# Performance work log

Hardware: AMD Instinct MI355X
Metric: run time of the kernel (lower is better)

## Reference

```python
import jax, jax.numpy as jnp
import numpy as np

B, N, NDIM = 256, 127, 3          # batch, particles, input features
D, H, L, HID = 256, 8, 4, 256     # d_model, heads, layers, dim_feedforward(=nb_features=head hidden)
M = HID                           # Performer nb_features
DH = D // H                       # head dim
LN_EPS = 1e-5
KERN_EPS = 1e-4


def leaky(x):
    return jnp.where(x >= 0, x, 0.2 * x)


def layer_norm(x, g, b):
    mu = jnp.mean(x, axis=-1, keepdims=True)
    var = jnp.mean((x - mu) ** 2, axis=-1, keepdims=True)
    return (x - mu) * jax.lax.rsqrt(var + LN_EPS) * g + b


def softmax_kernel(data, proj, is_query):
    # FAVOR+ positive softmax random features (performer_pytorch.softmax_kernel)
    # data [B,H,S,DH], proj [M,DH]
    normalizer = DH ** -0.25
    ratio = proj.shape[0] ** -0.5
    dd = jnp.einsum('bhnd,md->bhnm', data * normalizer, proj)
    diag = jnp.sum(data ** 2, axis=-1, keepdims=True) * 0.5 * (normalizer ** 2)
    if is_query:
        mx = jax.lax.stop_gradient(jnp.max(dd, axis=-1, keepdims=True))
    else:
        mx = jax.lax.stop_gradient(jnp.max(dd))
    return ratio * (jnp.exp(dd - diag - mx) + KERN_EPS)


def performer_attn(h, keep, Wq, bq, Wk, bk, Wv, bv, Wo, bo, proj):
    Bc, S, _ = h.shape
    def split(y):
        return y.reshape(Bc, S, H, DH).transpose(0, 2, 1, 3)  # [B,H,S,DH]
    q = split(jnp.einsum('bnd,ed->bne', h, Wq) + bq)
    k = split(jnp.einsum('bnd,ed->bne', h, Wk) + bk)
    v = split(jnp.einsum('bnd,ed->bne', h, Wv) + bv) * keep   # zero padded values
    qp = softmax_kernel(q, proj, True)    # [B,H,S,M]
    kp = softmax_kernel(k, proj, False)   # [B,H,S,M]
    ksum = jnp.sum(kp, axis=2)                                   # [B,H,M]
    d_inv = 1.0 / jnp.einsum('bhnm,bhm->bhn', qp, ksum)          # [B,H,S]
    ctx = jnp.einsum('bhnm,bhnd->bhmd', kp, v)                   # [B,H,M,DH]
    o = jnp.einsum('bhmd,bhnm,bhn->bhnd', ctx, qp, d_inv)
    o = o.transpose(0, 2, 1, 3).reshape(Bc, S, D)
    return jnp.einsum('bnd,ed->bne', o, Wo) + bo


def encoder_layer(h, keep, Wq, bq, Wk, bk, Wv, bv, Wo, bo, proj,
                  n1w, n1b, n2w, n2b, f1w, f1b, f2w, f2b):
    # NOTE: the repo's override drops the residual connections (post-norm, no skip)
    a = performer_attn(h, keep, Wq, bq, Wk, bk, Wv, bv, Wo, bo, proj)
    h = layer_norm(a, n1w, n1b)
    f = jnp.einsum('bnh,dh->bnd', leaky(jnp.einsum('bnd,hd->bnh', h, f1w) + f1b), f2w) + f2b
    return layer_norm(f, n2w, n2b)


def setup_inputs():
    key = jax.random.key(0)
    ks = jax.random.split(key, 32)
    s = 0.02
    def w(k, shape):
        return jax.random.normal(k, shape, jnp.float32) * s
    return {
        'x': jax.random.normal(ks[0], (B, N, NDIM), jnp.float32),
        'mask': jax.random.randint(ks[1], (B, N), 0, 2) == 1,
        'emb_w': w(ks[2], (D, NDIM)), 'emb_b': w(ks[3], (D,)),
        'Wq': w(ks[4], (L, D, D)), 'bq': w(ks[5], (L, D)),
        'Wk': w(ks[6], (L, D, D)), 'bk': w(ks[7], (L, D)),
        'Wv': w(ks[8], (L, D, D)), 'bv': w(ks[9], (L, D)),
        'Wo': w(ks[10], (L, D, D)), 'bo': w(ks[11], (L, D)),
        'proj': jax.random.normal(ks[12], (L, M, DH), jnp.float32),
        'n1w': jnp.ones((L, D)), 'n1b': jnp.zeros((L, D)),
        'n2w': jnp.ones((L, D)), 'n2b': jnp.zeros((L, D)),
        'f1w': w(ks[13], (L, HID, D)), 'f1b': w(ks[14], (L, HID)),
        'f2w': w(ks[15], (L, D, HID)), 'f2b': w(ks[16], (L, D)),
        'h1w': w(ks[17], (2 * HID, D)), 'h1b': w(ks[18], (2 * HID,)),
        'h2w': w(ks[19], (HID, 2 * HID)), 'h2b': w(ks[20], (HID,)),
        'ow': w(ks[21], (1, HID)), 'ob': w(ks[22], (1,)),
    }


def reference(x, mask, emb_w, emb_b, Wq, bq, Wk, bk, Wv, bv, Wo, bo, proj,
              n1w, n1b, n2w, n2b, f1w, f1b, f2w, f2b,
              h1w, h1b, h2w, h2b, ow, ob):
    h = jnp.einsum('bnf,df->bnd', x, emb_w) + emb_b               # embed [B,N,D]
    h = jnp.concatenate([jnp.zeros_like(h[:, :1]), h], axis=1)    # prepend zero CLS token
    pad = jnp.concatenate([jnp.zeros_like(mask[:, :1]), mask], axis=1)  # [B,N+1], True=pad
    keep = (~pad).astype(h.dtype)[:, None, :, None]               # [B,1,S,1]
    for l in range(L):
        h = encoder_layer(h, keep, Wq[l], bq[l], Wk[l], bk[l], Wv[l], bv[l],
                          Wo[l], bo[l], proj[l], n1w[l], n1b[l], n2w[l], n2b[l],
                          f1w[l], f1b[l], f2w[l], f2b[l])
    c = h[:, 0]                                                   # CLS token [B,D]
    c = leaky(jnp.einsum('bd,hd->bh', c, h1w) + h1b)
    c = leaky(jnp.einsum('bh,gh->bg', c, h2w) + h2b)
    return jnp.einsum('bg,og->bo', c, ow) + ob                    # [B,1]
```

## Files before the change

### kernel.cpp

```cpp
#include <hip/hip_runtime.h>
#include <math.h>

#define B_ 256
#define N_ 127
#define S_ 128
#define NDIM_ 3
#define D_ 256
#define H_ 8
#define DH_ 32
#define M_ 256
#define HID_ 256
#define L_ 4
#define LOG2E 1.44269504088896340736f

typedef __attribute__((ext_vector_type(8))) short short8;
typedef __attribute__((ext_vector_type(4))) short bfx4;
typedef __attribute__((ext_vector_type(4))) float floatx4;

__device__ __forceinline__ ushort bf16_rn(float x) {
    unsigned u = __float_as_uint(x);
    u = (u + 0x7fffu + ((u >> 16) & 1u)) >> 16;
    return (ushort)u;
}
__device__ __forceinline__ unsigned split_pack(float x) {
    const ushort h = bf16_rn(x);
    const float r = x - __uint_as_float(((unsigned)h) << 16);
    const ushort l = bf16_rn(r);
    return (unsigned)h | ((unsigned)l << 16);
}
__device__ __forceinline__ float rec(unsigned u) {
    return __uint_as_float(u << 16) + __uint_as_float(u & 0xffff0000u);
}
__device__ __forceinline__ unsigned hpair(unsigned u0, unsigned u1) {
    return (u0 & 0xffffu) | (u1 << 16);
}
__device__ __forceinline__ unsigned lpair(unsigned u0, unsigned u1) {
    return (u0 >> 16) | (u1 & 0xffff0000u);
}

__device__ __forceinline__ float blk_sum(float v, float* sred) {
#pragma unroll
    for (int o = 32; o > 0; o >>= 1) v += __shfl_xor(v, o, 64);
    if ((threadIdx.x & 63) == 0) sred[threadIdx.x >> 6] = v;
    __syncthreads();
    v = sred[0] + sred[1] + sred[2] + sred[3];
    __syncthreads();
    return v;
}

__global__ void __launch_bounds__(256) k_prep(
    const float* __restrict__ Wq, const float* __restrict__ Wk, const float* __restrict__ Wv,
    const float* __restrict__ Wo, const float* __restrict__ f1w, const float* __restrict__ f2w,
    const float* __restrict__ proj, ushort* __restrict__ WH, ushort* __restrict__ WL,
    unsigned* __restrict__ P2, int* __restrict__ slots,
    const float* __restrict__ x, const float* __restrict__ ew, const float* __restrict__ eb,
    unsigned* __restrict__ Aout)
{
    const int bid = blockIdx.x;
    if (bid < 768) {
        const int tensor = bid / 128;
        const int tid = (bid & 127) * 256 + threadIdx.x;
        const float* src = tensor == 0 ? Wq : tensor == 1 ? Wk : tensor == 2 ? Wv
                         : tensor == 3 ? Wo : tensor == 4 ? f1w : f2w;
        ushort* dh = WH + (size_t)tensor * L_ * 65536;
        ushort* dl = WL + (size_t)tensor * L_ * 65536;
        const int l = tid >> 13;
        const int col = (tid >> 5) & 255, kc = tid & 31;
        const float* sp = src + ((size_t)l << 16) + col * 256 + kc * 8;
        float v[8];
        *(float4*)&v[0] = *(const float4*)sp;
        *(float4*)&v[4] = *(const float4*)(sp + 4);
        unsigned hu[4], lu[4];
#pragma unroll
        for (int i = 0; i < 4; i++) {
            const unsigned u0 = split_pack(v[2 * i]);
            const unsigned u1 = split_pack(v[2 * i + 1]);
            hu[i] = hpair(u0, u1);
            lu[i] = lpair(u0, u1);
        }
        const size_t off = ((size_t)l << 16) + ((size_t)(kc * 256 + col)) * 8;
        *(uint4*)&dh[off] = make_uint4(hu[0], hu[1], hu[2], hu[3]);
        *(uint4*)&dl[off] = make_uint4(lu[0], lu[1], lu[2], lu[3]);
    } else if (bid < 800) {
        const int idx = ((bid - 768) * 256 + threadIdx.x) * 4;
        const float4 w4 = *(const float4*)&proj[idx];
        const float v[4] = {w4.x, w4.y, w4.z, w4.w};
        unsigned u[4];
#pragma unroll
        for (int i = 0; i < 4; i++) u[i] = split_pack(v[i]);
        *(uint4*)&P2[idx] = make_uint4(u[0], u[1], u[2], u[3]);
    } else if (bid == 800) {
        if (threadIdx.x < 4) {
            const int i = __float_as_int(-INFINITY);
            slots[threadIdx.x] = (i >= 0) ? i : (i ^ 0x7fffffff);
        }
    } else {
        const int idx4 = (bid - 801) * 256 + threadIdx.x;
        const int d0 = (idx4 & 63) * 4;
        const int n = (idx4 >> 6) & (S_ - 1);
        const int b = idx4 >> 13;
        unsigned r[4] = {0u, 0u, 0u, 0u};
        if (n > 0) {
            const float* xr = x + ((size_t)b * N_ + (n - 1)) * NDIM_;
            const float x0 = xr[0], x1 = xr[1], x2 = xr[2];
#pragma unroll
            for (int j = 0; j < 4; j++) {
                const int d = d0 + j;
                const float val = eb[d] + x0 * ew[d * 3 + 0] + x1 * ew[d * 3 + 1] + x2 * ew[d * 3 + 2];
                r[j] = split_pack(val);
            }
        }
        *(uint4*)&Aout[(size_t)idx4 * 4] = make_uint4(r[0], r[1], r[2], r[3]);
    }
}

template<int EPI>
__global__ void __launch_bounds__(512, 2) k_gemm(
    const unsigned* __restrict__ Ap, const ushort* __restrict__ WH,
    const ushort* __restrict__ WL,
    const float* __restrict__ bias, const float* __restrict__ g1,
    const float* __restrict__ g2, const int* __restrict__ mask,
    unsigned* __restrict__ out)
{
    __shared__ ushort sAh[2][4160];
    __shared__ ushort sAl[2][4160];
    __shared__ float sredA[128][4], sredB[128][4];
    const int t = threadIdx.x;
    const int w = t >> 6, lane = t & 63;
    const int quad = lane >> 4, l16 = lane & 15;
    const int rowbase = 64 * (w >> 2), colbase = 64 * (w & 3);
    const int colg = w & 3;
    const int row0 = blockIdx.x * 128;

    floatx4 acc[4][4];
#pragma unroll
    for (int rt = 0; rt < 4; rt++)
#pragma unroll
        for (int ct = 0; ct < 4; ct++) acc[rt][ct] = (floatx4){0.f, 0.f, 0.f, 0.f};

    const int arow = t >> 2, achunk = t & 3;
    const unsigned* AG = Ap + (size_t)(row0 + arow) * D_ + achunk * 8;
    const int aidx = achunk * 1040 + arow * 8;

    {
        const uint4 a0 = *(const uint4*)AG;
        const uint4 a1 = *(const uint4*)(AG + 4);
        *(uint4*)&sAh[0][aidx] = make_uint4(hpair(a0.x, a0.y), hpair(a0.z, a0.w),
                                            hpair(a1.x, a1.y), hpair(a1.z, a1.w));
        *(uint4*)&sAl[0][aidx] = make_uint4(lpair(a0.x, a0.y), lpair(a0.z, a0.w),
                                            lpair(a1.x, a1.y), lpair(a1.z, a1.w));
    }
    __syncthreads();

    for (int s = 0; s < 8; s++) {
        const int p = s & 1;
        uint4 a0n, a1n;
        if (s + 1 < 8) {
            a0n = *(const uint4*)(AG + (s + 1) * 32);
            a1n = *(const uint4*)(AG + (s + 1) * 32 + 4);
        }
        const size_t wbase = ((size_t)((s * 4 + quad) * 256 + colbase + l16)) * 8;
        const ushort* WHf = WH + wbase;
        const ushort* WLf = WL + wbase;
        short8 ah[4], al[4], wh[4], wl[4];
#pragma unroll
        for (int ct = 0; ct < 4; ct++) {
            wh[ct] = *(const short8*)&WHf[ct * 128];
            wl[ct] = *(const short8*)&WLf[ct * 128];
        }
#pragma unroll
        for (int rt = 0; rt < 4; rt++) {
            const int ai = quad * 1040 + (rowbase + 16 * rt + l16) * 8;
            ah[rt] = *(const short8*)&sAh[p][ai];
            al[rt] = *(const short8*)&sAl[p][ai];
        }
#pragma unroll
        for (int rt = 0; rt < 4; rt++)
#pragma unroll
            for (int ct = 0; ct < 4; ct++) {
                acc[rt][ct] = __builtin_amdgcn_mfma_f32_16x16x32_bf16(ah[rt], wh[ct], acc[rt][ct], 0, 0, 0);
                acc[rt][ct] = __builtin_amdgcn_mfma_f32_16x16x32_bf16(ah[rt], wl[ct], acc[rt][ct], 0, 0, 0);
                acc[rt][ct] = __builtin_amdgcn_mfma_f32_16x16x32_bf16(al[rt], wh[ct], acc[rt][ct], 0, 0, 0);
            }
        if (s + 1 < 8) {
            *(uint4*)&sAh[p ^ 1][aidx] = make_uint4(hpair(a0n.x, a0n.y), hpair(a0n.z, a0n.w),
                                                    hpair(a1n.x, a1n.y), hpair(a1n.z, a1n.w));
            *(uint4*)&sAl[p ^ 1][aidx] = make_uint4(lpair(a0n.x, a0n.y), lpair(a0n.z, a0n.w),
                                                    lpair(a1n.x, a1n.y), lpair(a1n.z, a1n.w));
        }
        __syncthreads();
    }

    int colv[4]; float bv[4];
#pragma unroll
    for (int ct = 0; ct < 4; ct++) { colv[ct] = colbase + 16 * ct + l16; bv[ct] = bias[colv[ct]]; }

    if (EPI <= 1) {
        const int b = row0 >> 7;
#pragma unroll
        for (int rt = 0; rt < 4; rt++)
#pragma unroll
        for (int i = 0; i < 4; i++) {
            const int rl = rowbase + 16 * rt + quad * 4 + i;
            const int n = (row0 + rl) & (S_ - 1);
            float keep = 1.f;
            if (EPI == 1) keep = (n == 0) ? 1.f : (mask[b * N_ + n - 1] ? 0.f : 1.f);
#pragma unroll
            for (int ct = 0; ct < 4; ct++) {
                float c = acc[rt][ct][i] + bv[ct];
                if (EPI == 1) c *= keep;
                const int col = colv[ct];
                out[(((size_t)b * H_ + (col >> 5)) * S_ + n) * DH_ + (col & 31)] = split_pack(c);
            }
        }
    } else if (EPI == 2) {
        float gv[4], bbv[4];
#pragma unroll
        for (int ct = 0; ct < 4; ct++) { gv[ct] = g1[colv[ct]]; bbv[ct] = g2[colv[ct]]; }
#pragma unroll
        for (int rt = 0; rt < 4; rt++)
#pragma unroll
        for (int i = 0; i < 4; i++) {
            const int rl = rowbase + 16 * rt + quad * 4 + i;
            float s = 0.f, s2 = 0.f;
#pragma unroll
            for (int ct = 0; ct < 4; ct++) {
                const float c = acc[rt][ct][i] + bv[ct];
                s += c; s2 += c * c;
            }
#pragma unroll
            for (int o = 8; o > 0; o >>= 1) { s += __shfl_xor(s, o, 64); s2 += __shfl_xor(s2, o, 64); }
            if (l16 == 0) { sredA[rl][colg] = s; sredB[rl][colg] = s2; }
        }
        __syncthreads();
#pragma unroll
        for (int rt = 0; rt < 4; rt++)
#pragma unroll
        for (int i = 0; i < 4; i++) {
            const int rl = rowbase + 16 * rt + quad * 4 + i;
            const float s = sredA[rl][0] + sredA[rl][1] + sredA[rl][2] + sredA[rl][3];
            const float s2 = sredB[rl][0] + sredB[rl][1] + sredB[rl][2] + sredB[rl][3];
            const float mu = s * (1.f / D_);
            const float rs = rsqrtf(s2 * (1.f / D_) - mu * mu + 1e-5f);
#pragma unroll
            for (int ct = 0; ct < 4; ct++) {
                const float c = acc[rt][ct][i] + bv[ct];
                out[(size_t)(row0 + rl) * D_ + colv[ct]] = split_pack((c - mu) * rs * gv[ct] + bbv[ct]);
            }
        }
    } else {
#pragma unroll
        for (int rt = 0; rt < 4; rt++)
#pragma unroll
        for (int i = 0; i < 4; i++) {
            const int rl = rowbase + 16 * rt + quad * 4 + i;
#pragma unroll
            for (int ct = 0; ct < 4; ct++) {
                const float c = acc[rt][ct][i] + bv[ct];
                out[(size_t)(row0 + rl) * D_ + colv[ct]] = split_pack((c >= 0.f) ? c : 0.2f * c);
            }
        }
    }
}

__global__ void __launch_bounds__(512, 2) k_gemm_qkv(
    const unsigned* __restrict__ Ap, const ushort* __restrict__ WHb,
    const ushort* __restrict__ WLb, const int l,
    const float* __restrict__ bq, const float* __restrict__ bk, const float* __restrict__ bv_,
    const int* __restrict__ mask,
    unsigned* __restrict__ Qo, unsigned* __restrict__ Ko, unsigned* __restrict__ Vo)
{
    __shared__ ushort sAh[2][4160];
    __shared__ ushort sAl[2][4160];
    const int t = threadIdx.x;
    const int w = t >> 6, lane = t & 63;
    const int quad = lane >> 4, l16 = lane & 15;
    const int rowbase = 64 * (w >> 2), colbase = 64 * (w & 3);
    const int which = blockIdx.x >> 8;
    const int row0 = (blockIdx.x & 255) * 128;
    const ushort* WH = WHb + ((size_t)(which * L_ + l)) * 65536;
    const ushort* WL = WLb + ((size_t)(which * L_ + l)) * 65536;
    const float* bias = which == 0 ? bq : which == 1 ? bk : bv_;
    unsigned* out = which == 0 ? Qo : which == 1 ? Ko : Vo;

    floatx4 acc[4][4];
#pragma unroll
    for (int rt = 0; rt < 4; rt++)
#pragma unroll
        for (int ct = 0; ct < 4; ct++) acc[rt][ct] = (floatx4){0.f, 0.f, 0.f, 0.f};

    const int arow = t >> 2, achunk = t & 3;
    const unsigned* AG = Ap + (size_t)(row0 + arow) * D_ + achunk * 8;
    const int aidx = achunk * 1040 + arow * 8;

    {
        const uint4 a0 = *(const uint4*)AG;
        const uint4 a1 = *(const uint4*)(AG + 4);
        *(uint4*)&sAh[0][aidx] = make_uint4(hpair(a0.x, a0.y), hpair(a0.z, a0.w),
                                            hpair(a1.x, a1.y), hpair(a1.z, a1.w));
        *(uint4*)&sAl[0][aidx] = make_uint4(lpair(a0.x, a0.y), lpair(a0.z, a0.w),
                                            lpair(a1.x, a1.y), lpair(a1.z, a1.w));
    }
    __syncthreads();

    for (int s = 0; s < 8; s++) {
        const int p = s & 1;
        uint4 a0n, a1n;
        if (s + 1 < 8) {
            a0n = *(const uint4*)(AG + (s + 1) * 32);
            a1n = *(const uint4*)(AG + (s + 1) * 32 + 4);
        }
        const size_t wbase = ((size_t)((s * 4 + quad) * 256 + colbase + l16)) * 8;
        const ushort* WHf = WH + wbase;
        const ushort* WLf = WL + wbase;
        short8 ah[4], al[4], wh[4], wl[4];
#pragma unroll
        for (int ct = 0; ct < 4; ct++) {
            wh[ct] = *(const short8*)&WHf[ct * 128];
            wl[ct] = *(const short8*)&WLf[ct * 128];
        }
#pragma unroll
        for (int rt = 0; rt < 4; rt++) {
            const int ai = quad * 1040 + (rowbase + 16 * rt + l16) * 8;
            ah[rt] = *(const short8*)&sAh[p][ai];
            al[rt] = *(const short8*)&sAl[p][ai];
        }
#pragma unroll
        for (int rt = 0; rt < 4; rt++)
#pragma unroll
            for (int ct = 0; ct < 4; ct++) {
                acc[rt][ct] = __builtin_amdgcn_mfma_f32_16x16x32_bf16(ah[rt], wh[ct], acc[rt][ct], 0, 0, 0);
                acc[rt][ct] = __builtin_amdgcn_mfma_f32_16x16x32_bf16(ah[rt], wl[ct], acc[rt][ct], 0, 0, 0);
                acc[rt][ct] = __builtin_amdgcn_mfma_f32_16x16x32_bf16(al[rt], wh[ct], acc[rt][ct], 0, 0, 0);
            }
        if (s + 1 < 8) {
            *(uint4*)&sAh[p ^ 1][aidx] = make_uint4(hpair(a0n.x, a0n.y), hpair(a0n.z, a0n.w),
                                                    hpair(a1n.x, a1n.y), hpair(a1n.z, a1n.w));
            *(uint4*)&sAl[p ^ 1][aidx] = make_uint4(lpair(a0n.x, a0n.y), lpair(a0n.z, a0n.w),
                                                    lpair(a1n.x, a1n.y), lpair(a1n.z, a1n.w));
        }
        __syncthreads();
    }

    int colv[4]; float bv[4];
#pragma unroll
    for (int ct = 0; ct < 4; ct++) { colv[ct] = colbase + 16 * ct + l16; bv[ct] = bias[colv[ct]]; }

    const int b = row0 >> 7;
#pragma unroll
    for (int rt = 0; rt < 4; rt++)
#pragma unroll
    for (int i = 0; i < 4; i++) {
        const int rl = rowbase + 16 * rt + quad * 4 + i;
        const int n = (row0 + rl) & (S_ - 1);
        float keep = 1.f;
        if (which == 2) keep = (n == 0) ? 1.f : (mask[b * N_ + n - 1] ? 0.f : 1.f);
#pragma unroll
        for (int ct = 0; ct < 4; ct++) {
            float c = acc[rt][ct][i] + bv[ct];
            c *= keep;
            const int col = colv[ct];
            out[(((size_t)b * H_ + (col >> 5)) * S_ + n) * DH_ + (col & 31)] = split_pack(c);
        }
    }
}

__global__ void __launch_bounds__(512, 4) k_ffn(
    const unsigned* __restrict__ Ap,
    const ushort* __restrict__ W1H, const ushort* __restrict__ W1L,
    const ushort* __restrict__ W2H, const ushort* __restrict__ W2L,
    const float* __restrict__ b1, const float* __restrict__ b2,
    const float* __restrict__ g1, const float* __restrict__ g2,
    unsigned* __restrict__ out)
{
    __shared__ char smemc[67584];
    ushort* h1h = (ushort*)smemc;
    ushort* h1l = (ushort*)(smemc + 33792);
    ushort* sTh = (ushort*)smemc;
    ushort* sTl = (ushort*)(smemc + 8320);
    __shared__ float sredA[64][4], sredB[64][4];
    const int t = threadIdx.x;
    const int w = t >> 6, lane = t & 63;
    const int quad = lane >> 4, l16 = lane & 15;
    const int row0 = blockIdx.x * 64;

    floatx4 acc[2][4];
#pragma unroll
    for (int rt = 0; rt < 2; rt++)
#pragma unroll
        for (int ct = 0; ct < 4; ct++) acc[rt][ct] = (floatx4){0.f, 0.f, 0.f, 0.f};

    const int arow = t >> 3, akq = t & 7;
    const unsigned* AG = Ap + (size_t)(row0 + arow) * D_ + akq * 4;
    const int aidx = (akq >> 1) * 520 + arow * 8 + (akq & 1) * 4;

    {
        const uint4 a4 = *(const uint4*)AG;
        *(uint2*)&sTh[aidx] = make_uint2(hpair(a4.x, a4.y), hpair(a4.z, a4.w));
        *(uint2*)&sTl[aidx] = make_uint2(lpair(a4.x, a4.y), lpair(a4.z, a4.w));
    }
    __syncthreads();

    for (int s = 0; s < 8; s++) {
        const int p = s & 1;
        uint4 a_n;
        if (s + 1 < 8) a_n = *(const uint4*)(AG + (s + 1) * 32);
        const size_t wbase = ((size_t)((s * 4 + quad) * 256 + 32 * w + l16)) * 8;
        short8 fh[2], fl[2], th[4], tl[4];
#pragma unroll
        for (int rt = 0; rt < 2; rt++) {
            fh[rt] = *(const short8*)&W1H[wbase + rt * 128];
            fl[rt] = *(const short8*)&W1L[wbase + rt * 128];
        }
#pragma unroll
        for (int ct = 0; ct < 4; ct++) {
            const int ti = p * 2080 + quad * 520 + (16 * ct + l16) * 8;
            th[ct] = *(const short8*)&sTh[ti];
            tl[ct] = *(const short8*)&sTl[ti];
        }
#pragma unroll
        for (int rt = 0; rt < 2; rt++)
#pragma unroll
            for (int ct = 0; ct < 4; ct++) {
                acc[rt][ct] = __builtin_amdgcn_mfma_f32_16x16x32_bf16(fh[rt], th[ct], acc[rt][ct], 0, 0, 0);
                acc[rt][ct] = __builtin_amdgcn_mfma_f32_16x16x32_bf16(fl[rt], th[ct], acc[rt][ct], 0, 0, 0);
                acc[rt][ct] = __builtin_amdgcn_mfma_f32_16x16x32_bf16(fh[rt], tl[ct], acc[rt][ct], 0, 0, 0);
            }
        if (s + 1 < 8) {
            *(uint2*)&sTh[(p ^ 1) * 2080 + aidx] = make_uint2(hpair(a_n.x, a_n.y), hpair(a_n.z, a_n.w));
            *(uint2*)&sTl[(p ^ 1) * 2080 + aidx] = make_uint2(lpair(a_n.x, a_n.y), lpair(a_n.z, a_n.w));
        }
        __syncthreads();
    }
#pragma unroll
    for (int rt = 0; rt < 2; rt++)
#pragma unroll
    for (int ct = 0; ct < 4; ct++) {
        unsigned u[4];
#pragma unroll
        for (int i = 0; i < 4; i++) {
            const int col2 = 32 * w + 16 * rt + quad * 4 + i;
            float c = acc[rt][ct][i] + b1[col2];
            c = (c >= 0.f) ? c : 0.2f * c;
            u[i] = split_pack(c);
        }
        const int base = (16 * ct + l16) * 264 + 32 * w + 16 * rt + quad * 4;
        *(uint2*)&h1h[base] = make_uint2(hpair(u[0], u[1]), hpair(u[2], u[3]));
        *(uint2*)&h1l[base] = make_uint2(lpair(u[0], u[1]), lpair(u[2], u[3]));
    }
    __syncthreads();

    const int rowbase = 32 * (w >> 2), colbase = 64 * (w & 3);
    const int colg = w & 3;
    floatx4 acc2[2][4];
#pragma unroll
    for (int rt = 0; rt < 2; rt++)
#pragma unroll
        for (int ct = 0; ct < 4; ct++) acc2[rt][ct] = (floatx4){0.f, 0.f, 0.f, 0.f};

    for (int ks = 0; ks < 8; ks++) {
        const size_t w2base = ((size_t)((ks * 4 + quad) * 256 + colbase + l16)) * 8;
        short8 ah[2], al[2], wh[4], wl[4];
#pragma unroll
        for (int ct = 0; ct < 4; ct++) {
            wh[ct] = *(const short8*)&W2H[w2base + ct * 128];
            wl[ct] = *(const short8*)&W2L[w2base + ct * 128];
        }
#pragma unroll
        for (int rt = 0; rt < 2; rt++) {
            const int gi = (rowbase + 16 * rt + l16) * 264 + ks * 32 + quad * 8;
            ah[rt] = *(const short8*)&h1h[gi];
            al[rt] = *(const short8*)&h1l[gi];
        }
#pragma unroll
        for (int rt = 0; rt < 2; rt++)
#pragma unroll
            for (int ct = 0; ct < 4; ct++) {
                acc2[rt][ct] = __builtin_amdgcn_mfma_f32_16x16x32_bf16(ah[rt], wh[ct], acc2[rt][ct], 0, 0, 0);
                acc2[rt][ct] = __builtin_amdgcn_mfma_f32_16x16x32_bf16(ah[rt], wl[ct], acc2[rt][ct], 0, 0, 0);
                acc2[rt][ct] = __builtin_amdgcn_mfma_f32_16x16x32_bf16(al[rt], wh[ct], acc2[rt][ct], 0, 0, 0);
            }
    }
    __syncthreads();

    int colv[4]; float bv[4], gv[4], bbv[4];
#pragma unroll
    for (int ct = 0; ct < 4; ct++) {
        colv[ct] = colbase + 16 * ct + l16;
        bv[ct] = b2[colv[ct]];
        gv[ct] = g1[colv[ct]];
        bbv[ct] = g2[colv[ct]];
    }
#pragma unroll
    for (int rt = 0; rt < 2; rt++)
#pragma unroll
    for (int i = 0; i < 4; i++) {
        const int rl = rowbase + 16 * rt + quad * 4 + i;
        float s = 0.f, s2 = 0.f;
#pragma unroll
        for (int ct = 0; ct < 4; ct++) {
            const float c = acc2[rt][ct][i] + bv[ct];
            s += c; s2 += c * c;
        }
#pragma unroll
        for (int o = 8; o > 0; o >>= 1) { s += __shfl_xor(s, o, 64); s2 += __shfl_xor(s2, o, 64); }
        if (l16 == 0) { sredA[rl][colg] = s; sredB[rl][colg] = s2; }
    }
    __syncthreads();
#pragma unroll
    for (int rt = 0; rt < 2; rt++)
#pragma unroll
    for (int i = 0; i < 4; i++) {
        const int rl = rowbase + 16 * rt + quad * 4 + i;
        const float s = sredA[rl][0] + sredA[rl][1] + sredA[rl][2] + sredA[rl][3];
        const float s2 = sredB[rl][0] + sredB[rl][1] + sredB[rl][2] + sredB[rl][3];
        const float mu = s * (1.f / D_);
        const float rs = rsqrtf(s2 * (1.f / D_) - mu * mu + 1e-5f);
#pragma unroll
        for (int ct = 0; ct < 4; ct++) {
            const float c = acc2[rt][ct][i] + bv[ct];
            out[(size_t)(row0 + rl) * D_ + colv[ct]] = split_pack((c - mu) * rs * gv[ct] + bbv[ct]);
        }
    }
}

__global__ void __launch_bounds__(256) k_dmax(
    const unsigned* __restrict__ kg, const unsigned* __restrict__ P2, int* __restrict__ slot)
{
    __shared__ __align__(16) ushort A2s[64 * 40];
    __shared__ __align__(16) ushort Ps[256 * 40];
    __shared__ float sred[4];
    const int t = threadIdx.x;
    const size_t row0 = (size_t)blockIdx.x * 64;
    {
        const int row = t >> 2, seg = t & 3;
        const unsigned* src = kg + (row0 + row) * DH_ + seg * 8;
        const uint4 f0 = *(const uint4*)src;
        const uint4 f1 = *(const uint4*)(src + 4);
        *(uint4*)&A2s[row * 40 + seg * 8] =
            make_uint4(hpair(f0.x, f0.y), hpair(f0.z, f0.w), hpair(f1.x, f1.y), hpair(f1.z, f1.w));
    }
    {
        const int col = t;
        const unsigned* src = P2 + (size_t)col * DH_;
#pragma unroll
        for (int hf = 0; hf < 2; hf++) {
            const uint4 g0 = *(const uint4*)(src + hf * 16);
            const uint4 g1 = *(const uint4*)(src + hf * 16 + 4);
            const uint4 g2 = *(const uint4*)(src + hf * 16 + 8);
            const uint4 g3 = *(const uint4*)(src + hf * 16 + 12);
            *(uint4*)&Ps[col * 40 + hf * 16] =
                make_uint4(hpair(g0.x, g0.y), hpair(g0.z, g0.w), hpair(g1.x, g1.y), hpair(g1.z, g1.w));
            *(uint4*)&Ps[col * 40 + hf * 16 + 8] =
                make_uint4(hpair(g2.x, g2.y), hpair(g2.z, g2.w), hpair(g3.x, g3.y), hpair(g3.z, g3.w));
        }
    }
    __syncthreads();
    const int w = t >> 6, lane = t & 63, quad = lane >> 4, l16 = lane & 15;
    floatx4 acc[4][4];
#pragma unroll
    for (int rt = 0; rt < 4; rt++)
#pragma unroll
        for (int ct = 0; ct < 4; ct++) acc[rt][ct] = (floatx4){0.f, 0.f, 0.f, 0.f};
    short8 af[4], bf[4];
#pragma unroll
    for (int rt = 0; rt < 4; rt++)
        af[rt] = *(const short8*)&A2s[(rt * 16 + l16) * 40 + quad * 8];
#pragma unroll
    for (int ct = 0; ct < 4; ct++)
        bf[ct] = *(const short8*)&Ps[((w * 4 + ct) * 16 + l16) * 40 + quad * 8];
#pragma unroll
    for (int rt = 0; rt < 4; rt++)
#pragma unroll
        for (int ct = 0; ct < 4; ct++)
            acc[rt][ct] = __builtin_amdgcn_mfma_f32_16x16x32_bf16(af[rt], bf[ct], acc[rt][ct], 0, 0, 0);
    float mx = -INFINITY;
#pragma unroll
    for (int rt = 0; rt < 4; rt++)
#pragma unroll
        for (int ct = 0; ct < 4; ct++)
#pragma unroll
            for (int i = 0; i < 4; i++) mx = fmaxf(mx, acc[rt][ct][i]);
#pragma unroll
    for (int o = 32; o > 0; o >>= 1) mx = fmaxf(mx, __shfl_xor(mx, o, 64));
    if (lane == 0) sred[w] = mx;
    __syncthreads();
    if (t == 0) {
        const float m4 = fmaxf(fmaxf(sred[0], sred[1]), fmaxf(sred[2], sred[3]))
                       * 0.42044820762685725f;
        const int i = __float_as_int(m4);
        atomicMax(slot, (i >= 0) ? i : (i ^ 0x7fffffff));
    }
}

__global__ void __launch_bounds__(1024) k_attn2(
    const unsigned* __restrict__ qg, const unsigned* __restrict__ kg, const unsigned* __restrict__ vg,
    const unsigned* __restrict__ P2, const int* __restrict__ slot,
    unsigned* __restrict__ outp)
{
    extern __shared__ char smem[];
    ushort* sAh   = (ushort*)(smem);
    ushort* sAl   = (ushort*)(smem + 10240);
    ushort* sBh   = (ushort*)(smem + 20480);
    ushort* sBl   = (ushort*)(smem + 25600);
    ushort* kpS   = (ushort*)(smem + 30720);
    ushort* sV    = (ushort*)(smem + 48128);
    ushort* sCtx  = (ushort*)(smem + 56832);
    float* sdk    = (float*)(smem + 73728);
    float* sdq    = (float*)(smem + 74240);
    float* smaxP  = (float*)(smem + 74752);
    float* sdenP  = smaxP;
    float* sksum  = (float*)(smem + 75776);
    float* sksP   = (float*)(smem + 76800);

    const int bh = blockIdx.x;
    const int b = bh >> 3, hh = bh & 7;
    const int t = threadIdx.x;
    const int w = t >> 6, lane = t & 63, quad = lane >> 4, l16 = lane & 15;
    const int wg = w & 7, wh = w >> 3;
    const int nq = wg * 16 + l16;
    const unsigned* kb = kg + (size_t)bh * S_ * DH_;
    const unsigned* qb = qg + (size_t)bh * S_ * DH_;
    const unsigned* vb = vg + (size_t)bh * S_ * DH_;
    const float nrm = 0.42044820762685725f;
    const float diagc = 0.5f * nrm * nrm;
    const float ratio = 0.0625f;

    union U8 { uint4 u; short8 s; };
    union U4 { uint2 u; bfx4 s; };

    float kmaxv;
    { const int iv = *slot; kmaxv = __int_as_float((iv >= 0) ? iv : (iv ^ 0x7fffffff)); }

    short8 qfh, qfl;
    {
        const unsigned* qrow = qb + (size_t)nq * DH_ + quad * 8;
        const uint4 q0 = *(const uint4*)qrow;
        const uint4 q1 = *(const uint4*)(qrow + 4);
        U8 th; th.u = make_uint4(hpair(q0.x, q0.y), hpair(q0.z, q0.w), hpair(q1.x, q1.y), hpair(q1.z, q1.w));
        U8 tl; tl.u = make_uint4(lpair(q0.x, q0.y), lpair(q0.z, q0.w), lpair(q1.x, q1.y), lpair(q1.z, q1.w));
        qfh = th.s; qfl = tl.s;
    }

    if (t < 512) {
        const int row = t >> 2, seg = t & 3;
        const unsigned* src = kb + row * DH_ + seg * 8;
        const uint4 f0 = *(const uint4*)&src[0];
        const uint4 f1 = *(const uint4*)&src[4];
        *(uint4*)&sAh[row * 40 + seg * 8] =
            make_uint4(hpair(f0.x, f0.y), hpair(f0.z, f0.w), hpair(f1.x, f1.y), hpair(f1.z, f1.w));
        *(uint4*)&sAl[row * 40 + seg * 8] =
            make_uint4(lpair(f0.x, f0.y), lpair(f0.z, f0.w), lpair(f1.x, f1.y), lpair(f1.z, f1.w));
    } else {
        const int tt2 = t - 512;
        const int n = tt2 & 127, d0 = (tt2 >> 7) * 8;
        const unsigned* src = vb + n * DH_ + d0;
        const uint4 f0 = *(const uint4*)&src[0];
        const uint4 f1 = *(const uint4*)&src[4];
        const unsigned uu[8] = {f0.x, f0.y, f0.z, f0.w, f1.x, f1.y, f1.z, f1.w};
#pragma unroll
        for (int j = 0; j < 8; j++)
            sV[(d0 + j) * 136 + n] = (ushort)(uu[j] & 0xffffu);
    }
    if (t < 128) {
        float s = 0.f, s2 = 0.f;
#pragma unroll
        for (int d4 = 0; d4 < DH_ / 4; d4++) {
            const uint4 kk = *(const uint4*)&kb[t * DH_ + d4 * 4];
            const float k0 = rec(kk.x), k1 = rec(kk.y), k2 = rec(kk.z), k3 = rec(kk.w);
            s += k0 * k0 + k1 * k1 + k2 * k2 + k3 * k3;
            const uint4 qq = *(const uint4*)&qb[t * DH_ + d4 * 4];
            const float q0 = rec(qq.x), q1 = rec(qq.y), q2 = rec(qq.z), q3 = rec(qq.w);
            s2 += q0 * q0 + q1 * q1 + q2 * q2 + q3 * q3;
        }
        sdk[t] = s * diagc + kmaxv;
        sdq[t] = s2 * diagc;
    }
    __syncthreads();

    floatx4 adq[2][4];
#pragma unroll
    for (int j = 0; j < 2; j++)
#pragma unroll
        for (int mtl = 0; mtl < 4; mtl++) adq[j][mtl] = (floatx4){0.f, 0.f, 0.f, 0.f};

#pragma unroll
    for (int qd = 0; qd < 4; qd++) {
        {
            const int col = t >> 4, ch2 = t & 15;
            const unsigned* src = P2 + (size_t)(qd * 64 + col) * DH_ + ch2 * 2;
            const unsigned u0 = src[0], u1 = src[1];
            ((unsigned*)sBh)[col * 20 + ch2] = hpair(u0, u1);
            ((unsigned*)sBl)[col * 20 + ch2] = lpair(u0, u1);
        }
        __syncthreads();
        floatx4 acc[2];
        acc[0] = (floatx4){0.f, 0.f, 0.f, 0.f};
        acc[1] = (floatx4){0.f, 0.f, 0.f, 0.f};
        {
            const short8 afh = *(const short8*)&sAh[nq * 40 + quad * 8];
            const short8 afl = *(const short8*)&sAl[nq * 40 + quad * 8];
#pragma unroll
            for (int ctl = 0; ctl < 2; ctl++) {
                const int mrow = ((2 * wh + ctl) * 16 + l16) * 40 + quad * 8;
                const short8 bfh = *(const short8*)&sBh[mrow];
                const short8 bfl = *(const short8*)&sBl[mrow];
                acc[ctl] = __builtin_amdgcn_mfma_f32_16x16x32_bf16(afh, bfh, acc[ctl], 0, 0, 0);
                acc[ctl] = __builtin_amdgcn_mfma_f32_16x16x32_bf16(afh, bfl, acc[ctl], 0, 0, 0);
                acc[ctl] = __builtin_amdgcn_mfma_f32_16x16x32_bf16(afl, bfh, acc[ctl], 0, 0, 0);
            }
        }
        float kc[2];
#pragma unroll
        for (int ctl = 0; ctl < 2; ctl++) {
            float kcl = 0.f;
            ushort kh[4];
#pragma unroll
            for (int i = 0; i < 4; i++) {
                const int n = wg * 16 + quad * 4 + i;
                const float kp = ratio * (__expf(acc[ctl][i] * nrm - sdk[n]) + 1e-4f);
                kh[i] = bf16_rn(kp);
                kcl += __uint_as_float((unsigned)kh[i] << 16);
            }
            *(uint2*)&kpS[((2 * wh + ctl) * 16 + l16) * 136 + wg * 16 + quad * 4] =
                make_uint2((unsigned)kh[0] | ((unsigned)kh[1] << 16),
                           (unsigned)kh[2] | ((unsigned)kh[3] << 16));
            kc[ctl] = kcl;
        }
#pragma unroll
        for (int ctl = 0; ctl < 2; ctl++) {
            kc[ctl] += __shfl_xor(kc[ctl], 16, 64);
            kc[ctl] += __shfl_xor(kc[ctl], 32, 64);
        }
        if (quad == 0) {
            sksP[w * 32 + l16] = kc[0];
            sksP[w * 32 + 16 + l16] = kc[1];
        }
        __syncthreads();
        const int qown = (qd & 1) ^ 1;
        if (wh == qown) {
            const int aidx2 = qd >> 1;
#pragma unroll
            for (int mtl = 0; mtl < 4; mtl++) {
                const int prow = (mtl * 16 + l16) * 40 + quad * 8;
                const short8 aPh = *(const short8*)&sBh[prow];
                const short8 aPl = *(const short8*)&sBl[prow];
                adq[aidx2][mtl] = __builtin_amdgcn_mfma_f32_16x16x32_bf16(aPh, qfh, adq[aidx2][mtl], 0, 0, 0);
                adq[aidx2][mtl] = __builtin_amdgcn_mfma_f32_16x16x32_bf16(aPh, qfl, adq[aidx2][mtl], 0, 0, 0);
                adq[aidx2][mtl] = __builtin_amdgcn_mfma_f32_16x16x32_bf16(aPl, qfh, adq[aidx2][mtl], 0, 0, 0);
            }
        } else {
            const int mt = wg & 3, dt = wg >> 2;
            floatx4 cacc = (floatx4){0.f, 0.f, 0.f, 0.f};
#pragma unroll
            for (int ks = 0; ks < 4; ks++) {
                const short8 a = *(const short8*)&kpS[(mt * 16 + l16) * 136 + ks * 32 + quad * 8];
                const short8 bvv = *(const short8*)&sV[(dt * 16 + l16) * 136 + ks * 32 + quad * 8];
                cacc = __builtin_amdgcn_mfma_f32_16x16x32_bf16(a, bvv, cacc, 0, 0, 0);
            }
            ushort ch[4];
#pragma unroll
            for (int i = 0; i < 4; i++) ch[i] = bf16_rn(cacc[i]);
            *(uint2*)&sCtx[(dt * 16 + l16) * 264 + qd * 64 + mt * 16 + quad * 4] =
                make_uint2((unsigned)ch[0] | ((unsigned)ch[1] << 16),
                           (unsigned)ch[2] | ((unsigned)ch[3] << 16));
        }
        if (t < 64) {
            float s = 0.f;
#pragma unroll
            for (int wg2 = 0; wg2 < 8; wg2++)
                s += sksP[((t >> 5) * 8 + wg2) * 32 + (t & 31)];
            sksum[qd * 64 + t] = s;
        }
        __syncthreads();
    }

    {
        float mxn = -INFINITY;
#pragma unroll
        for (int j = 0; j < 2; j++)
#pragma unroll
            for (int mtl = 0; mtl < 4; mtl++)
#pragma unroll
                for (int i = 0; i < 4; i++) mxn = fmaxf(mxn, adq[j][mtl][i]);
        mxn = fmaxf(mxn, __shfl_xor(mxn, 16, 64));
        mxn = fmaxf(mxn, __shfl_xor(mxn, 32, 64));
        if (quad == 0) smaxP[wh * 128 + nq] = mxn;
    }
    __syncthreads();
    const float dmq = sdq[nq] + fmaxf(smaxP[nq], smaxP[128 + nq]) * nrm;

    floatx4 oT[2];
    oT[0] = (floatx4){0.f, 0.f, 0.f, 0.f};
    oT[1] = (floatx4){0.f, 0.f, 0.f, 0.f};
    float dp = 0.f;
#pragma unroll
    for (int j = 0; j < 2; j++) {
        const int qdo = 2 * j + (wh ^ 1);
#pragma unroll
        for (int mtl = 0; mtl < 4; mtl++) {
            ushort qh[4];
#pragma unroll
            for (int i = 0; i < 4; i++) {
                const float qp = ratio * (__expf(adq[j][mtl][i] * nrm - dmq) + 1e-4f);
                qh[i] = bf16_rn(qp);
                dp += __uint_as_float((unsigned)qh[i] << 16)
                    * sksum[qdo * 64 + mtl * 16 + quad * 4 + i];
            }
            U4 tb;
            tb.u = make_uint2((unsigned)qh[0] | ((unsigned)qh[1] << 16),
                              (unsigned)qh[2] | ((unsigned)qh[3] << 16));
#pragma unroll
            for (int dt = 0; dt < 2; dt++) {
                U4 ta;
                ta.u = *(const uint2*)&sCtx[(dt * 16 + l16) * 264 + qdo * 64 + mtl * 16 + quad * 4];
                oT[dt] = __builtin_amdgcn_mfma_f32_16x16x16bf16_1k(ta.s, tb.s, oT[dt], 0, 0, 0);
            }
        }
    }
    dp += __shfl_xor(dp, 16, 64);
    dp += __shfl_xor(dp, 32, 64);
    __syncthreads();
    if (quad == 0) sdenP[wh * 128 + nq] = dp;

    float* oRed = (float*)kpS;
    if (wh == 1) {
#pragma unroll
        for (int dt = 0; dt < 2; dt++)
            *(floatx4*)&oRed[((wg * 2 + dt) * 64 + lane) * 4] = oT[dt];
    }
    __syncthreads();
    if (wh == 0) {
        const float inv = 1.0f / (sdenP[nq] + sdenP[128 + nq]);
#pragma unroll
        for (int dt = 0; dt < 2; dt++) {
            const floatx4 o2 = *(const floatx4*)&oRed[((wg * 2 + dt) * 64 + lane) * 4];
            const unsigned r0 = split_pack((oT[dt][0] + o2[0]) * inv);
            const unsigned r1 = split_pack((oT[dt][1] + o2[1]) * inv);
            const unsigned r2 = split_pack((oT[dt][2] + o2[2]) * inv);
            const unsigned r3 = split_pack((oT[dt][3] + o2[3]) * inv);
            *(uint4*)&outp[((size_t)b * S_ + nq) * D_ + hh * DH_ + dt * 16 + quad * 4] =
                make_uint4(r0, r1, r2, r3);
        }
    }
}

__global__ void __launch_bounds__(256) k_head(
    const unsigned* __restrict__ hfin, const float* __restrict__ h1w, const float* __restrict__ h1b,
    const float* __restrict__ h2w, const float* __restrict__ h2b,
    const float* __restrict__ ow, const float* __restrict__ ob, float* __restrict__ outp)
{
    __shared__ float c0[D_];
    __shared__ float c1[2 * HID_];
    __shared__ float sred[4];
    const int t = threadIdx.x;
    const int b = blockIdx.x;
    c0[t] = rec(hfin[(size_t)b * S_ * D_ + t]);
    __syncthreads();
#pragma unroll
    for (int half = 0; half < 2; half++) {
        const int j = half * 256 + t;
        float a = h1b[j];
        const float* w = h1w + (size_t)j * D_;
        for (int d = 0; d < D_; d += 4) {
            const float4 w4 = *(const float4*)&w[d];
            const float4 x4 = *(const float4*)&c0[d];
            a += x4.x * w4.x + x4.y * w4.y + x4.z * w4.z + x4.w * w4.w;
        }
        c1[j] = (a >= 0.f) ? a : 0.2f * a;
    }
    __syncthreads();
    float a2 = h2b[t];
    const float* w2 = h2w + (size_t)t * (2 * HID_);
    for (int j = 0; j < 2 * HID_; j += 4) {
        const float4 w4 = *(const float4*)&w2[j];
        const float4 x4 = *(const float4*)&c1[j];
        a2 += x4.x * w4.x + x4.y * w4.y + x4.z * w4.z + x4.w * w4.w;
    }
    const float c2 = (a2 >= 0.f) ? a2 : 0.2f * a2;
    const float s = blk_sum(c2 * ow[t], sred);
    if (t == 0) outp[b] = s + ob[0];
}

extern "C" void kernel_launch(void* const* d_in, const int* in_sizes, int n_in,
                              void* d_out, int out_size, void* d_ws, size_t ws_size,
                              hipStream_t stream)
{
    const float* x     = (const float*)d_in[0];
    const int*   mask  = (const int*)d_in[1];
    const float* emb_w = (const float*)d_in[2];
    const float* emb_b = (const float*)d_in[3];
    const float* Wq    = (const float*)d_in[4];
    const float* bq    = (const float*)d_in[5];
    const float* Wk    = (const float*)d_in[6];
    const float* bk    = (const float*)d_in[7];
    const float* Wv    = (const float*)d_in[8];
    const float* bv    = (const float*)d_in[9];
    const float* Wo    = (const float*)d_in[10];
    const float* bo    = (const float*)d_in[11];
    const float* proj  = (const float*)d_in[12];
    const float* n1w   = (const float*)d_in[13];
    const float* n1b   = (const float*)d_in[14];
    const float* n2w   = (const float*)d_in[15];
    const float* n2b   = (const float*)d_in[16];
    const float* f1w   = (const float*)d_in[17];
    const float* f1b   = (const float*)d_in[18];
    const float* f2w   = (const float*)d_in[19];
    const float* f2b   = (const float*)d_in[20];
    const float* h1w   = (const float*)d_in[21];
    const float* h1b   = (const float*)d_in[22];
    const float* h2w   = (const float*)d_in[23];
    const float* h2b   = (const float*)d_in[24];
    const float* ow    = (const float*)d_in[25];
    const float* ob    = (const float*)d_in[26];

    const size_t BSD = (size_t)B_ * S_ * D_;
    unsigned* A = (unsigned*)d_ws;
    unsigned* Q = A + BSD;
    unsigned* K = Q + BSD;
    unsigned* V = K + BSD;
    unsigned* T = K;
    const size_t WMU = 65536;
    ushort* WH = (ushort*)(V + BSD);
    ushort* WL = WH + 6 * L_ * WMU;
    unsigned* P2 = (unsigned*)(WL + 6 * L_ * WMU);
    int* slots = (int*)(P2 + (size_t)L_ * M_ * DH_);

    k_prep<<<801 + 8192, 256, 0, stream>>>(Wq, Wk, Wv, Wo, f1w, f2w, proj, WH, WL, P2, slots,
                                           x, emb_w, emb_b, A);

    const int GB2 = B_ * S_ / 128;
    const int DB = B_ * H_ * S_ / 64;
    const size_t ATTN_LDS = 78848;

    for (int l = 0; l < L_; l++) {
        const unsigned* P2l = P2 + (size_t)l * M_ * DH_;
        k_gemm_qkv<<<3 * GB2, 512, 0, stream>>>(A, WH, WL, l, bq + l * D_, bk + l * D_, bv + l * D_, mask, Q, K, V);
        k_dmax<<<DB, 256, 0, stream>>>(K, P2l, slots + l);
        k_attn2<<<B_ * H_, 1024, ATTN_LDS, stream>>>(Q, K, V, P2l, slots + l, A);
        k_gemm<2><<<GB2, 512, 0, stream>>>(A, WH + (3 * L_ + l) * WMU, WL + (3 * L_ + l) * WMU, bo + l * D_, n1w + l * D_, n1b + l * D_, nullptr, T);
        k_ffn<<<B_ * S_ / 64, 512, 0, stream>>>(T, WH + (4 * L_ + l) * WMU, WL + (4 * L_ + l) * WMU,
                                      WH + (5 * L_ + l) * WMU, WL + (5 * L_ + l) * WMU,
                                      f1b + l * HID_, f2b + l * D_, n2w + l * D_, n2b + l * D_, A);
    }
    k_head<<<B_, 256, 0, stream>>>(A, h1w, h1b, h2w, h2b, ow, ob, (float*)d_out);
}
```

Baseline: 1.216 ms.

## Fuse output projection and LayerNorm into FFN kernel

Merges the attention output projection (Wo + bias + LayerNorm1) into the FFN kernel, so each 64-row tile computes Wo, normalizes in LDS, then runs FFN1 and FFN2 without writing the intermediate T to global memory. This removes one kernel launch per layer and a full global round-trip of the post-attention activation. In exchange, occupancy drops (launch bounds go from 4 to 2 blocks per CU), the kernel does more sequential work, and the in-place write to A reads and writes the same buffer, which is safe only if each block touches only its own rows.

```diff
diff --git a/kernel.cpp b/kernel.cpp
--- a/kernel.cpp
+++ b/kernel.cpp
@@ -114,155 +114,6 @@
     }
 }
 
-template<int EPI>
-__global__ void __launch_bounds__(512, 2) k_gemm(
-    const unsigned* __restrict__ Ap, const ushort* __restrict__ WH,
-    const ushort* __restrict__ WL,
-    const float* __restrict__ bias, const float* __restrict__ g1,
-    const float* __restrict__ g2, const int* __restrict__ mask,
-    unsigned* __restrict__ out)
-{
-    __shared__ ushort sAh[2][4160];
-    __shared__ ushort sAl[2][4160];
-    __shared__ float sredA[128][4], sredB[128][4];
-    const int t = threadIdx.x;
-    const int w = t >> 6, lane = t & 63;
-    const int quad = lane >> 4, l16 = lane & 15;
-    const int rowbase = 64 * (w >> 2), colbase = 64 * (w & 3);
-    const int colg = w & 3;
-    const int row0 = blockIdx.x * 128;
-
-    floatx4 acc[4][4];
-#pragma unroll
-    for (int rt = 0; rt < 4; rt++)
-#pragma unroll
-        for (int ct = 0; ct < 4; ct++) acc[rt][ct] = (floatx4){0.f, 0.f, 0.f, 0.f};
-
-    const int arow = t >> 2, achunk = t & 3;
-    const unsigned* AG = Ap + (size_t)(row0 + arow) * D_ + achunk * 8;
-    const int aidx = achunk * 1040 + arow * 8;
-
-    {
-        const uint4 a0 = *(const uint4*)AG;
-        const uint4 a1 = *(const uint4*)(AG + 4);
-        *(uint4*)&sAh[0][aidx] = make_uint4(hpair(a0.x, a0.y), hpair(a0.z, a0.w),
-                                            hpair(a1.x, a1.y), hpair(a1.z, a1.w));
-        *(uint4*)&sAl[0][aidx] = make_uint4(lpair(a0.x, a0.y), lpair(a0.z, a0.w),
-                                            lpair(a1.x, a1.y), lpair(a1.z, a1.w));
-    }
-    __syncthreads();
-
-    for (int s = 0; s < 8; s++) {
-        const int p = s & 1;
-        uint4 a0n, a1n;
-        if (s + 1 < 8) {
-            a0n = *(const uint4*)(AG + (s + 1) * 32);
-            a1n = *(const uint4*)(AG + (s + 1) * 32 + 4);
-        }
-        const size_t wbase = ((size_t)((s * 4 + quad) * 256 + colbase + l16)) * 8;
-        const ushort* WHf = WH + wbase;
-        const ushort* WLf = WL + wbase;
-        short8 ah[4], al[4], wh[4], wl[4];
-#pragma unroll
-        for (int ct = 0; ct < 4; ct++) {
-            wh[ct] = *(const short8*)&WHf[ct * 128];
-            wl[ct] = *(const short8*)&WLf[ct * 128];
-        }
-#pragma unroll
-        for (int rt = 0; rt < 4; rt++) {
-            const int ai = quad * 1040 + (rowbase + 16 * rt + l16) * 8;
-            ah[rt] = *(const short8*)&sAh[p][ai];
-            al[rt] = *(const short8*)&sAl[p][ai];
-        }
-#pragma unroll
-        for (int rt = 0; rt < 4; rt++)
-#pragma unroll
-            for (int ct = 0; ct < 4; ct++) {
-                acc[rt][ct] = __builtin_amdgcn_mfma_f32_16x16x32_bf16(ah[rt], wh[ct], acc[rt][ct], 0, 0, 0);
-                acc[rt][ct] = __builtin_amdgcn_mfma_f32_16x16x32_bf16(ah[rt], wl[ct], acc[rt][ct], 0, 0, 0);
-                acc[rt][ct] = __builtin_amdgcn_mfma_f32_16x16x32_bf16(al[rt], wh[ct], acc[rt][ct], 0, 0, 0);
-            }
-        if (s + 1 < 8) {
-            *(uint4*)&sAh[p ^ 1][aidx] = make_uint4(hpair(a0n.x, a0n.y), hpair(a0n.z, a0n.w),
-                                                    hpair(a1n.x, a1n.y), hpair(a1n.z, a1n.w));
-            *(uint4*)&sAl[p ^ 1][aidx] = make_uint4(lpair(a0n.x, a0n.y), lpair(a0n.z, a0n.w),
-                                                    lpair(a1n.x, a1n.y), lpair(a1n.z, a1n.w));
-        }
-        __syncthreads();
-    }
-
-    int colv[4]; float bv[4];
-#pragma unroll
-    for (int ct = 0; ct < 4; ct++) { colv[ct] = colbase + 16 * ct + l16; bv[ct] = bias[colv[ct]]; }
-
-    if (EPI <= 1) {
-        const int b = row0 >> 7;
-#pragma unroll
-        for (int rt = 0; rt < 4; rt++)
-#pragma unroll
-        for (int i = 0; i < 4; i++) {
-            const int rl = rowbase + 16 * rt + quad * 4 + i;
-            const int n = (row0 + rl) & (S_ - 1);
-            float keep = 1.f;
-            if (EPI == 1) keep = (n == 0) ? 1.f : (mask[b * N_ + n - 1] ? 0.f : 1.f);
-#pragma unroll
-            for (int ct = 0; ct < 4; ct++) {
-                float c = acc[rt][ct][i] + bv[ct];
-                if (EPI == 1) c *= keep;
-                const int col = colv[ct];
-                out[(((size_t)b * H_ + (col >> 5)) * S_ + n) * DH_ + (col & 31)] = split_pack(c);
-            }
-        }
-    } else if (EPI == 2) {
-        float gv[4], bbv[4];
-#pragma unroll
-        for (int ct = 0; ct < 4; ct++) { gv[ct] = g1[colv[ct]]; bbv[ct] = g2[colv[ct]]; }
-#pragma unroll
-        for (int rt = 0; rt < 4; rt++)
-#pragma unroll
-        for (int i = 0; i < 4; i++) {
-            const int rl = rowbase + 16 * rt + quad * 4 + i;
-            float s = 0.f, s2 = 0.f;
-#pragma unroll
-            for (int ct = 0; ct < 4; ct++) {
-                const float c = acc[rt][ct][i] + bv[ct];
-                s += c; s2 += c * c;
-            }
-#pragma unroll
-            for (int o = 8; o > 0; o >>= 1) { s += __shfl_xor(s, o, 64); s2 += __shfl_xor(s2, o, 64); }
-            if (l16 == 0) { sredA[rl][colg] = s; sredB[rl][colg] = s2; }
-        }
-        __syncthreads();
-#pragma unroll
-        for (int rt = 0; rt < 4; rt++)
-#pragma unroll
-        for (int i = 0; i < 4; i++) {
-            const int rl = rowbase + 16 * rt + quad * 4 + i;
-            const float s = sredA[rl][0] + sredA[rl][1] + sredA[rl][2] + sredA[rl][3];
-            const float s2 = sredB[rl][0] + sredB[rl][1] + sredB[rl][2] + sredB[rl][3];
-            const float mu = s * (1.f / D_);
-            const float rs = rsqrtf(s2 * (1.f / D_) - mu * mu + 1e-5f);
-#pragma unroll
-            for (int ct = 0; ct < 4; ct++) {
-                const float c = acc[rt][ct][i] + bv[ct];
-                out[(size_t)(row0 + rl) * D_ + colv[ct]] = split_pack((c - mu) * rs * gv[ct] + bbv[ct]);
-            }
-        }
-    } else {
-#pragma unroll
-        for (int rt = 0; rt < 4; rt++)
-#pragma unroll
-        for (int i = 0; i < 4; i++) {
-            const int rl = rowbase + 16 * rt + quad * 4 + i;
-#pragma unroll
-            for (int ct = 0; ct < 4; ct++) {
-                const float c = acc[rt][ct][i] + bv[ct];
-                out[(size_t)(row0 + rl) * D_ + colv[ct]] = split_pack((c >= 0.f) ? c : 0.2f * c);
-            }
-        }
-    }
-}
-
 __global__ void __launch_bounds__(512, 2) k_gemm_qkv(
     const unsigned* __restrict__ Ap, const ushort* __restrict__ WHb,
     const ushort* __restrict__ WLb, const int l,
@@ -365,20 +216,22 @@
     }
 }
 
-__global__ void __launch_bounds__(512, 4) k_ffn(
+__global__ void __launch_bounds__(512, 2) k_wofn(
     const unsigned* __restrict__ Ap,
+    const ushort* __restrict__ WoH, const ushort* __restrict__ WoL,
     const ushort* __restrict__ W1H, const ushort* __restrict__ W1L,
     const ushort* __restrict__ W2H, const ushort* __restrict__ W2L,
+    const float* __restrict__ bo, const float* __restrict__ n1w, const float* __restrict__ n1b,
     const float* __restrict__ b1, const float* __restrict__ b2,
-    const float* __restrict__ g1, const float* __restrict__ g2,
+    const float* __restrict__ g2w, const float* __restrict__ g2b,
     unsigned* __restrict__ out)
 {
     __shared__ char smemc[67584];
-    ushort* h1h = (ushort*)smemc;
-    ushort* h1l = (ushort*)(smemc + 33792);
+    ushort* Th  = (ushort*)smemc;
+    ushort* Tl  = (ushort*)(smemc + 33792);
     ushort* sTh = (ushort*)smemc;
     ushort* sTl = (ushort*)(smemc + 8320);
-    __shared__ float sredA[64][4], sredB[64][4];
+    __shared__ float sredA[64][8], sredB[64][8];
     const int t = threadIdx.x;
     const int w = t >> 6, lane = t & 63;
     const int quad = lane >> 4, l16 = lane & 15;
@@ -409,8 +262,8 @@
         short8 fh[2], fl[2], th[4], tl[4];
 #pragma unroll
         for (int rt = 0; rt < 2; rt++) {
-            fh[rt] = *(const short8*)&W1H[wbase + rt * 128];
-            fl[rt] = *(const short8*)&W1L[wbase + rt * 128];
+            fh[rt] = *(const short8*)&WoH[wbase + rt * 128];
+            fl[rt] = *(const short8*)&WoL[wbase + rt * 128];
         }
 #pragma unroll
         for (int ct = 0; ct < 4; ct++) {
@@ -432,23 +285,133 @@
         }
         __syncthreads();
     }
+
+    {
+        float bov[2][4];
+#pragma unroll
+        for (int rt = 0; rt < 2; rt++)
+#pragma unroll
+            for (int i = 0; i < 4; i++) bov[rt][i] = bo[32 * w + 16 * rt + quad * 4 + i];
+        float ps[4], ps2[4];
+#pragma unroll
+        for (int ct = 0; ct < 4; ct++) { ps[ct] = 0.f; ps2[ct] = 0.f; }
+#pragma unroll
+        for (int rt = 0; rt < 2; rt++)
+#pragma unroll
+        for (int ct = 0; ct < 4; ct++)
+#pragma unroll
+        for (int i = 0; i < 4; i++) {
+            const float c = acc[rt][ct][i] + bov[rt][i];
+            acc[rt][ct][i] = c;
+            ps[ct] += c; ps2[ct] += c * c;
+        }
+#pragma unroll
+        for (int ct = 0; ct < 4; ct++) {
+            ps[ct] += __shfl_xor(ps[ct], 16, 64);  ps[ct] += __shfl_xor(ps[ct], 32, 64);
+            ps2[ct] += __shfl_xor(ps2[ct], 16, 64); ps2[ct] += __shfl_xor(ps2[ct], 32, 64);
+        }
+        if (quad == 0) {
+#pragma unroll
+            for (int ct = 0; ct < 4; ct++) {
+                sredA[16 * ct + l16][w] = ps[ct];
+                sredB[16 * ct + l16][w] = ps2[ct];
+            }
+        }
+        __syncthreads();
+        float mu[4], rs[4];
+#pragma unroll
+        for (int ct = 0; ct < 4; ct++) {
+            const int n = 16 * ct + l16;
+            float s = 0.f, s2 = 0.f;
+#pragma unroll
+            for (int k = 0; k < 8; k++) { s += sredA[n][k]; s2 += sredB[n][k]; }
+            mu[ct] = s * (1.f / D_);
+            rs[ct] = rsqrtf(s2 * (1.f / D_) - mu[ct] * mu[ct] + 1e-5f);
+        }
+        float gv1[2][4], bv1[2][4];
+#pragma unroll
+        for (int rt = 0; rt < 2; rt++)
+#pragma unroll
+            for (int i = 0; i < 4; i++) {
+                const int c2 = 32 * w + 16 * rt + quad * 4 + i;
+                gv1[rt][i] = n1w[c2];
+                bv1[rt][i] = n1b[c2];
+            }
+#pragma unroll
+        for (int ct = 0; ct < 4; ct++) {
+            const int n = 16 * ct + l16;
+#pragma unroll
+            for (int rt = 0; rt < 2; rt++) {
+                unsigned u[4];
+#pragma unroll
+                for (int i = 0; i < 4; i++) {
+                    const float tv = (acc[rt][ct][i] - mu[ct]) * rs[ct] * gv1[rt][i] + bv1[rt][i];
+                    u[i] = split_pack(tv);
+                }
+                const int base = n * 264 + 32 * w + 16 * rt + quad * 4;
+                *(uint2*)&Th[base] = make_uint2(hpair(u[0], u[1]), hpair(u[2], u[3]));
+                *(uint2*)&Tl[base] = make_uint2(lpair(u[0], u[1]), lpair(u[2], u[3]));
+            }
+        }
+        __syncthreads();
+    }
+
+    floatx4 acc1[2][4];
 #pragma unroll
     for (int rt = 0; rt < 2; rt++)
 #pragma unroll
-    for (int ct = 0; ct < 4; ct++) {
-        unsigned u[4];
-#pragma unroll
-        for (int i = 0; i < 4; i++) {
-            const int col2 = 32 * w + 16 * rt + quad * 4 + i;
-            float c = acc[rt][ct][i] + b1[col2];
-            c = (c >= 0.f) ? c : 0.2f * c;
-            u[i] = split_pack(c);
-        }
-        const int base = (16 * ct + l16) * 264 + 32 * w + 16 * rt + quad * 4;
-        *(uint2*)&h1h[base] = make_uint2(hpair(u[0], u[1]), hpair(u[2], u[3]));
-        *(uint2*)&h1l[base] = make_uint2(lpair(u[0], u[1]), lpair(u[2], u[3]));
-    }
-    __syncthreads();
+        for (int ct = 0; ct < 4; ct++) acc1[rt][ct] = (floatx4){0.f, 0.f, 0.f, 0.f};
+
+    for (int s = 0; s < 8; s++) {
+        const size_t wbase = ((size_t)((s * 4 + quad) * 256 + 32 * w + l16)) * 8;
+        short8 fh[2], fl[2], th[4], tl[4];
+#pragma unroll
+        for (int rt = 0; rt < 2; rt++) {
+            fh[rt] = *(const short8*)&W1H[wbase + rt * 128];
+            fl[rt] = *(const short8*)&W1L[wbase + rt * 128];
+        }
+#pragma unroll
+        for (int ct = 0; ct < 4; ct++) {
+            const int ti = (16 * ct + l16) * 264 + s * 32 + quad * 8;
+            th[ct] = *(const short8*)&Th[ti];
+            tl[ct] = *(const short8*)&Tl[ti];
+        }
+#pragma unroll
+        for (int rt = 0; rt < 2; rt++)
+#pragma unroll
+            for (int ct = 0; ct < 4; ct++) {
+                acc1[rt][ct] = __builtin_amdgcn_mfma_f32_16x16x32_bf16(fh[rt], th[ct], acc1[rt][ct], 0, 0, 0);
+                acc1[rt][ct] = __builtin_amdgcn_mfma_f32_16x16x32_bf16(fl[rt], th[ct], acc1[rt][ct], 0, 0, 0);
+                acc1[rt][ct] = __builtin_amdgcn_mfma_f32_16x16x32_bf16(fh[rt], tl[ct], acc1[rt][ct], 0, 0, 0);
+            }
+    }
+    __syncthreads();
+
+    {
+        float b1v[2][4];
+#pragma unroll
+        for (int rt = 0; rt < 2; rt++)
+#pragma unroll
+            for (int i = 0; i < 4; i++) b1v[rt][i] = b1[32 * w + 16 * rt + quad * 4 + i];
+#pragma unroll
+        for (int ct = 0; ct < 4; ct++) {
+            const int n = 16 * ct + l16;
+#pragma unroll
+            for (int rt = 0; rt < 2; rt++) {
+                unsigned u[4];
+#pragma unroll
+                for (int i = 0; i < 4; i++) {
+                    float c = acc1[rt][ct][i] + b1v[rt][i];
+                    c = (c >= 0.f) ? c : 0.2f * c;
+                    u[i] = split_pack(c);
+                }
+                const int base = n * 264 + 32 * w + 16 * rt + quad * 4;
+                *(uint2*)&Th[base] = make_uint2(hpair(u[0], u[1]), hpair(u[2], u[3]));
+                *(uint2*)&Tl[base] = make_uint2(lpair(u[0], u[1]), lpair(u[2], u[3]));
+            }
+        }
+        __syncthreads();
+    }
 
     const int rowbase = 32 * (w >> 2), colbase = 64 * (w & 3);
     const int colg = w & 3;
@@ -469,8 +432,8 @@
 #pragma unroll
         for (int rt = 0; rt < 2; rt++) {
             const int gi = (rowbase + 16 * rt + l16) * 264 + ks * 32 + quad * 8;
-            ah[rt] = *(const short8*)&h1h[gi];
-            al[rt] = *(const short8*)&h1l[gi];
+            ah[rt] = *(const short8*)&Th[gi];
+            al[rt] = *(const short8*)&Tl[gi];
         }
 #pragma unroll
         for (int rt = 0; rt < 2; rt++)
@@ -488,8 +451,8 @@
     for (int ct = 0; ct < 4; ct++) {
         colv[ct] = colbase + 16 * ct + l16;
         bv[ct] = b2[colv[ct]];
-        gv[ct] = g1[colv[ct]];
-        bbv[ct] = g2[colv[ct]];
+        gv[ct] = g2w[colv[ct]];
+        bbv[ct] = g2b[colv[ct]];
     }
 #pragma unroll
     for (int rt = 0; rt < 2; rt++)
@@ -919,7 +882,6 @@
     unsigned* Q = A + BSD;
     unsigned* K = Q + BSD;
     unsigned* V = K + BSD;
-    unsigned* T = K;
     const size_t WMU = 65536;
     ushort* WH = (ushort*)(V + BSD);
     ushort* WL = WH + 6 * L_ * WMU;
@@ -938,10 +900,12 @@
         k_gemm_qkv<<<3 * GB2, 512, 0, stream>>>(A, WH, WL, l, bq + l * D_, bk + l * D_, bv + l * D_, mask, Q, K, V);
         k_dmax<<<DB, 256, 0, stream>>>(K, P2l, slots + l);
         k_attn2<<<B_ * H_, 1024, ATTN_LDS, stream>>>(Q, K, V, P2l, slots + l, A);
-        k_gemm<2><<<GB2, 512, 0, stream>>>(A, WH + (3 * L_ + l) * WMU, WL + (3 * L_ + l) * WMU, bo + l * D_, n1w + l * D_, n1b + l * D_, nullptr, T);
-        k_ffn<<<B_ * S_ / 64, 512, 0, stream>>>(T, WH + (4 * L_ + l) * WMU, WL + (4 * L_ + l) * WMU,
-                                      WH + (5 * L_ + l) * WMU, WL + (5 * L_ + l) * WMU,
-                                      f1b + l * HID_, f2b + l * D_, n2w + l * D_, n2b + l * D_, A);
+        k_wofn<<<B_ * S_ / 64, 512, 0, stream>>>(A,
+            WH + (3 * L_ + l) * WMU, WL + (3 * L_ + l) * WMU,
+            WH + (4 * L_ + l) * WMU, WL + (4 * L_ + l) * WMU,
+            WH + (5 * L_ + l) * WMU, WL + (5 * L_ + l) * WMU,
+            bo + l * D_, n1w + l * D_, n1b + l * D_,
+            f1b + l * HID_, f2b + l * D_, n2w + l * D_, n2b + l * D_, A);
     }
     k_head<<<B_, 256, 0, stream>>>(A, h1w, h1b, h2w, h2b, ow, ob, (float*)d_out);
 }
```

Result: faster. 1.155 ms (median of 2 runs) (-5.0%).
